# Performance work log

Hardware: AMD Instinct MI355X
Metric: run time of the kernel (lower is better)

The kernel has to match this reference:

```python
import jax, jax.numpy as jnp
import numpy as np

N_NODES = 100000
N_EDGES = 1_600_000
IN_CH = 128
HIDDEN = 128


def gcn_conv(x, src, dst, W, b):
    """PyG-style GCNConv: self-loops + symmetric deg^{-1/2} normalization."""
    n = x.shape[0]
    xw = x @ W  # [N, H]
    # degree on destination after adding self-loops (each node gets +1)
    deg = jax.ops.segment_sum(jnp.ones(src.shape[0], dtype=xw.dtype), dst,
                              num_segments=n) + 1.0
    dinv = jax.lax.rsqrt(deg)                      # deg^{-1/2}
    norm = dinv[src] * dinv[dst]                   # per-edge norm [E]
    agg = jax.ops.segment_sum(xw[src] * norm[:, None], dst, num_segments=n)
    # self-loop contribution: norm_ii = deg_i^{-1}
    return agg + xw * (1.0 / deg)[:, None] + b


def setup_inputs() -> dict:
    key = jax.random.key(0)
    ks = jax.random.split(key, 10)
    s = 0.05
    return {
        "node_features": jax.random.normal(ks[0], (N_NODES, IN_CH), dtype=jnp.float32),
        "edge_index": jax.random.randint(ks[1], (2, N_EDGES), 0, N_NODES, dtype=jnp.int32),
        "W1": jax.random.normal(ks[2], (IN_CH, HIDDEN), dtype=jnp.float32) * s,
        "b1": jnp.zeros((HIDDEN,), dtype=jnp.float32),
        "W2": jax.random.normal(ks[3], (HIDDEN, HIDDEN), dtype=jnp.float32) * s,
        "b2": jnp.zeros((HIDDEN,), dtype=jnp.float32),
        "fc1_w": jax.random.normal(ks[4], (2 * HIDDEN, HIDDEN), dtype=jnp.float32) * s,
        "fc1_b": jnp.zeros((HIDDEN,), dtype=jnp.float32),
        "fc2_w": jax.random.normal(ks[5], (HIDDEN, 1), dtype=jnp.float32) * s,
        "fc2_b": jnp.zeros((1,), dtype=jnp.float32),
    }


def reference(node_features, edge_index, W1, b1, W2, b2, fc1_w, fc1_b, fc2_w, fc2_b):
    src, dst = edge_index[0], edge_index[1]
    # two GCN layers (dropout is identity in eval mode)
    h = jax.nn.relu(gcn_conv(node_features, src, dst, W1, b1))
    h = jax.nn.relu(gcn_conv(h, src, dst, W2, b2))
    # edge feature head: gather endpoints, elementwise product/difference
    x = h[src]  # [E, H]
    y = h[dst]  # [E, H]
    edge_features = jnp.concatenate([x * y, x - y], axis=1)  # [E, 2H]
    z = jax.nn.relu(edge_features @ fc1_w + fc1_b)
    prob = jax.nn.sigmoid(z @ fc2_w + fc2_b)  # [E, 1]
    return prob
```

## Files before the change

### kernel.cpp

```cpp
#include <hip/hip_runtime.h>

#define THREADS 256

typedef __bf16    bf16x8 __attribute__((ext_vector_type(8)));
typedef __bf16    bf16x4 __attribute__((ext_vector_type(4)));
typedef _Float16  f16x8  __attribute__((ext_vector_type(8)));
typedef float     f32x4  __attribute__((ext_vector_type(4)));


__global__ __launch_bounds__(THREADS) void k_hist(const int* __restrict__ dst,
                                                  int* __restrict__ cnt, int E) {
    int e = blockIdx.x * THREADS + threadIdx.x;
    if (e < E) atomicAdd(&cnt[dst[e]], 1);
}

__global__ __launch_bounds__(THREADS) void k_dinv(const int* __restrict__ cnt,
                                                  float* __restrict__ dinv, int n) {
    int i = blockIdx.x * THREADS + threadIdx.x;
    if (i < n) dinv[i] = rsqrtf((float)cnt[i] + 1.0f);
}

__global__ __launch_bounds__(THREADS) void k_scan1(const int* __restrict__ cnt,
                                                   int* __restrict__ rowptr,
                                                   int* __restrict__ blockSums, int n) {
    __shared__ int part[THREADS];
    int tid = threadIdx.x;
    int base = blockIdx.x * 1024 + tid * 4;
    int v0 = (base + 0 < n) ? cnt[base + 0] : 0;
    int v1 = (base + 1 < n) ? cnt[base + 1] : 0;
    int v2 = (base + 2 < n) ? cnt[base + 2] : 0;
    int v3 = (base + 3 < n) ? cnt[base + 3] : 0;
    part[tid] = v0 + v1 + v2 + v3;
    __syncthreads();
    for (int off = 1; off < THREADS; off <<= 1) {
        int t = 0;
        if (tid >= off) t = part[tid - off];
        __syncthreads();
        if (tid >= off) part[tid] += t;
        __syncthreads();
    }
    int excl = (tid == 0) ? 0 : part[tid - 1];
    if (tid == THREADS - 1) blockSums[blockIdx.x] = part[THREADS - 1];
    int run = excl;
    if (base + 0 < n) rowptr[base + 0] = run; run += v0;
    if (base + 1 < n) rowptr[base + 1] = run; run += v1;
    if (base + 2 < n) rowptr[base + 2] = run; run += v2;
    if (base + 3 < n) rowptr[base + 3] = run;
}

__global__ __launch_bounds__(THREADS) void k_scan2(int* __restrict__ blockSums,
                                                   int* __restrict__ rowptr,
                                                   int nchunks, int n, int E) {
    __shared__ int part[THREADS];
    int tid = threadIdx.x;
    int v = (tid < nchunks) ? blockSums[tid] : 0;
    part[tid] = v;
    __syncthreads();
    for (int off = 1; off < THREADS; off <<= 1) {
        int t = 0;
        if (tid >= off) t = part[tid - off];
        __syncthreads();
        if (tid >= off) part[tid] += t;
        __syncthreads();
    }
    int excl = (tid == 0) ? 0 : part[tid - 1];
    if (tid < nchunks) blockSums[tid] = excl;
    if (tid == 0) rowptr[n] = E;
}

__global__ __launch_bounds__(THREADS) void k_scan3(int* __restrict__ rowptr,
                                                   const int* __restrict__ blockSums, int n) {
    int i = blockIdx.x * THREADS + threadIdx.x;
    if (i < n) rowptr[i] += blockSums[i >> 10];
}

__global__ __launch_bounds__(THREADS) void k_scatter(const int* __restrict__ src,
                                                     const int* __restrict__ dst,
                                                     const int* __restrict__ rowptr,
                                                     const float* __restrict__ dinv,
                                                     int* __restrict__ cursor,
                                                     int2* __restrict__ swPair,
                                                     int2* __restrict__ sdSorted,
                                                     int* __restrict__ edgePerm, int E) {
    int e = blockIdx.x * THREADS + threadIdx.x;
    if (e >= E) return;
    int d = dst[e];
    int s = src[e];
    int pos = rowptr[d] + atomicAdd(&cursor[d], 1);
    swPair[pos] = make_int2(s, __float_as_int(dinv[s]));
    sdSorted[pos] = make_int2(s, d);
    edgePerm[pos] = e;
}

__global__ __launch_bounds__(THREADS) void k_gemm128_f32(const float* __restrict__ A,
                                                         const float* __restrict__ B,
                                                         float* __restrict__ C,
                                                         __bf16* __restrict__ C16, int M) {
    __shared__ float4 As[64][8];
    __shared__ float4 Bs[32][32];

    int tid = threadIdx.x;
    int tx = tid & 31;
    int ty = tid >> 5;
    int row0 = blockIdx.x * 64;

    float4 acc[8];
#pragma unroll
    for (int i = 0; i < 8; i++) acc[i] = make_float4(0.f, 0.f, 0.f, 0.f);

    for (int k0 = 0; k0 < 128; k0 += 32) {
#pragma unroll
        for (int i = 0; i < 2; i++) {
            int idx = tid + i * 256;
            int r = idx >> 3, q = idx & 7;
            int row = row0 + r;
            float4 v = make_float4(0.f, 0.f, 0.f, 0.f);
            if (row < M) v = *(const float4*)(A + (size_t)row * 128 + k0 + q * 4);
            As[r][q] = v;
        }
#pragma unroll
        for (int i = 0; i < 4; i++) {
            int idx = tid + i * 256;
            int r = idx >> 5, c4 = idx & 31;
            Bs[r][c4] = *(const float4*)(B + (size_t)(k0 + r) * 128 + c4 * 4);
        }
        __syncthreads();

#pragma unroll
        for (int k4 = 0; k4 < 8; k4++) {
            float4 b0 = Bs[k4 * 4 + 0][tx];
            float4 b1 = Bs[k4 * 4 + 1][tx];
            float4 b2 = Bs[k4 * 4 + 2][tx];
            float4 b3 = Bs[k4 * 4 + 3][tx];
#pragma unroll
            for (int i = 0; i < 8; i++) {
                float4 a = As[ty * 8 + i][k4];
                acc[i].x = fmaf(a.x, b0.x, fmaf(a.y, b1.x, fmaf(a.z, b2.x, fmaf(a.w, b3.x, acc[i].x))));
                acc[i].y = fmaf(a.x, b0.y, fmaf(a.y, b1.y, fmaf(a.z, b2.y, fmaf(a.w, b3.y, acc[i].y))));
                acc[i].z = fmaf(a.x, b0.z, fmaf(a.y, b1.z, fmaf(a.z, b2.z, fmaf(a.w, b3.z, acc[i].z))));
                acc[i].w = fmaf(a.x, b0.w, fmaf(a.y, b1.w, fmaf(a.z, b2.w, fmaf(a.w, b3.w, acc[i].w))));
            }
        }
        __syncthreads();
    }

#pragma unroll
    for (int i = 0; i < 8; i++) {
        int row = row0 + ty * 8 + i;
        if (row < M) {
            *(float4*)(C + (size_t)row * 128 + tx * 4) = acc[i];
            bf16x4 c16;
            c16[0] = (__bf16)acc[i].x; c16[1] = (__bf16)acc[i].y;
            c16[2] = (__bf16)acc[i].z; c16[3] = (__bf16)acc[i].w;
            *(bf16x4*)(C16 + (size_t)row * 128 + tx * 4) = c16;
        }
    }
}

__global__ __launch_bounds__(THREADS) void k_gemm128_f16(const _Float16* __restrict__ A,
                                                         const float* __restrict__ B,
                                                         float* __restrict__ C,
                                                         __bf16* __restrict__ C16, int M) {
    __shared__ float4 As[64][8];
    __shared__ float4 Bs[32][32];

    int tid = threadIdx.x;
    int tx = tid & 31;
    int ty = tid >> 5;
    int row0 = blockIdx.x * 64;

    float4 acc[8];
#pragma unroll
    for (int i = 0; i < 8; i++) acc[i] = make_float4(0.f, 0.f, 0.f, 0.f);

    for (int k0 = 0; k0 < 128; k0 += 32) {
        {
            int r = tid >> 2, q = tid & 3;
            int row = row0 + r;
            f16x8 v;
            if (row < M) v = *(const f16x8*)(A + (size_t)row * 128 + k0 + q * 8);
            else { f16x8 z = {}; v = z; }
            float4 lo = make_float4((float)v[0], (float)v[1], (float)v[2], (float)v[3]);
            float4 hi = make_float4((float)v[4], (float)v[5], (float)v[6], (float)v[7]);
            As[r][q * 2] = lo;
            As[r][q * 2 + 1] = hi;
        }
#pragma unroll
        for (int i = 0; i < 4; i++) {
            int idx = tid + i * 256;
            int r = idx >> 5, c4 = idx & 31;
            Bs[r][c4] = *(const float4*)(B + (size_t)(k0 + r) * 128 + c4 * 4);
        }
        __syncthreads();

#pragma unroll
        for (int k4 = 0; k4 < 8; k4++) {
            float4 b0 = Bs[k4 * 4 + 0][tx];
            float4 b1 = Bs[k4 * 4 + 1][tx];
            float4 b2 = Bs[k4 * 4 + 2][tx];
            float4 b3 = Bs[k4 * 4 + 3][tx];
#pragma unroll
            for (int i = 0; i < 8; i++) {
                float4 a = As[ty * 8 + i][k4];
                acc[i].x = fmaf(a.x, b0.x, fmaf(a.y, b1.x, fmaf(a.z, b2.x, fmaf(a.w, b3.x, acc[i].x))));
                acc[i].y = fmaf(a.x, b0.y, fmaf(a.y, b1.y, fmaf(a.z, b2.y, fmaf(a.w, b3.y, acc[i].y))));
                acc[i].z = fmaf(a.x, b0.z, fmaf(a.y, b1.z, fmaf(a.z, b2.z, fmaf(a.w, b3.z, acc[i].z))));
                acc[i].w = fmaf(a.x, b0.w, fmaf(a.y, b1.w, fmaf(a.z, b2.w, fmaf(a.w, b3.w, acc[i].w))));
            }
        }
        __syncthreads();
    }

#pragma unroll
    for (int i = 0; i < 8; i++) {
        int row = row0 + ty * 8 + i;
        if (row < M) {
            *(float4*)(C + (size_t)row * 128 + tx * 4) = acc[i];
            bf16x4 c16;
            c16[0] = (__bf16)acc[i].x; c16[1] = (__bf16)acc[i].y;
            c16[2] = (__bf16)acc[i].z; c16[3] = (__bf16)acc[i].w;
            *(bf16x4*)(C16 + (size_t)row * 128 + tx * 4) = c16;
        }
    }
}

__global__ __launch_bounds__(THREADS) void k_gather_agg(const int* __restrict__ rowptr,
                                                        const int2* __restrict__ swPair,
                                                        const __bf16* __restrict__ xw16,
                                                        const float* __restrict__ xw,
                                                        const float* __restrict__ dinv,
                                                        const float* __restrict__ bias,
                                                        _Float16* __restrict__ h16, int n) {
    int node = blockIdx.x * 4 + (threadIdx.x >> 6);
    int lane = threadIdx.x & 63;
    int q = lane >> 4;
    int c = lane & 15;
    if (node >= n) return;
    int beg = rowptr[node], end = rowptr[node + 1];
    float di = dinv[node];

    float acc[8];
#pragma unroll
    for (int i = 0; i < 8; i++) acc[i] = 0.f;

    int j = beg;
    for (; j + 15 < end; j += 16) {
        int2 pw0 = swPair[j + q];
        int2 pw1 = swPair[j + 4 + q];
        int2 pw2 = swPair[j + 8 + q];
        int2 pw3 = swPair[j + 12 + q];
        bf16x8 v0 = *(const bf16x8*)(xw16 + (size_t)pw0.x * 128 + c * 8);
        bf16x8 v1 = *(const bf16x8*)(xw16 + (size_t)pw1.x * 128 + c * 8);
        bf16x8 v2 = *(const bf16x8*)(xw16 + (size_t)pw2.x * 128 + c * 8);
        bf16x8 v3 = *(const bf16x8*)(xw16 + (size_t)pw3.x * 128 + c * 8);
        float w0 = __int_as_float(pw0.y);
        float w1 = __int_as_float(pw1.y);
        float w2 = __int_as_float(pw2.y);
        float w3 = __int_as_float(pw3.y);
#pragma unroll
        for (int i = 0; i < 8; i++) {
            acc[i] = fmaf((float)v0[i], w0, acc[i]);
            acc[i] = fmaf((float)v1[i], w1, acc[i]);
            acc[i] = fmaf((float)v2[i], w2, acc[i]);
            acc[i] = fmaf((float)v3[i], w3, acc[i]);
        }
    }
    for (; j + 7 < end; j += 8) {
        int2 pw0 = swPair[j + q];
        int2 pw1 = swPair[j + 4 + q];
        bf16x8 v0 = *(const bf16x8*)(xw16 + (size_t)pw0.x * 128 + c * 8);
        bf16x8 v1 = *(const bf16x8*)(xw16 + (size_t)pw1.x * 128 + c * 8);
        float w0 = __int_as_float(pw0.y);
        float w1 = __int_as_float(pw1.y);
#pragma unroll
        for (int i = 0; i < 8; i++) {
            acc[i] = fmaf((float)v0[i], w0, acc[i]);
            acc[i] = fmaf((float)v1[i], w1, acc[i]);
        }
    }
    for (; j + 3 < end; j += 4) {
        int2 pw = swPair[j + q];
        bf16x8 v = *(const bf16x8*)(xw16 + (size_t)pw.x * 128 + c * 8);
        float w = __int_as_float(pw.y);
#pragma unroll
        for (int i = 0; i < 8; i++) acc[i] = fmaf((float)v[i], w, acc[i]);
    }
    int rem = end - j;
    if (q < rem) {
        int2 pw = swPair[j + q];
        bf16x8 v = *(const bf16x8*)(xw16 + (size_t)pw.x * 128 + c * 8);
        float w = __int_as_float(pw.y);
#pragma unroll
        for (int i = 0; i < 8; i++) acc[i] = fmaf((float)v[i], w, acc[i]);
    }

#pragma unroll
    for (int i = 0; i < 8; i++) {
        acc[i] += __shfl_xor(acc[i], 16);
        acc[i] += __shfl_xor(acc[i], 32);
    }

    if (q == 0) {
        float4 xv0 = *(const float4*)(xw + (size_t)node * 128 + c * 8);
        float4 xv1 = *(const float4*)(xw + (size_t)node * 128 + c * 8 + 4);
        float4 b0 = *(const float4*)(bias + c * 8);
        float4 b1 = *(const float4*)(bias + c * 8 + 4);
        float dd = di * di;
        float r[8];
        r[0] = fmaxf(fmaf(acc[0], di, fmaf(xv0.x, dd, b0.x)), 0.f);
        r[1] = fmaxf(fmaf(acc[1], di, fmaf(xv0.y, dd, b0.y)), 0.f);
        r[2] = fmaxf(fmaf(acc[2], di, fmaf(xv0.z, dd, b0.z)), 0.f);
        r[3] = fmaxf(fmaf(acc[3], di, fmaf(xv0.w, dd, b0.w)), 0.f);
        r[4] = fmaxf(fmaf(acc[4], di, fmaf(xv1.x, dd, b1.x)), 0.f);
        r[5] = fmaxf(fmaf(acc[5], di, fmaf(xv1.y, dd, b1.y)), 0.f);
        r[6] = fmaxf(fmaf(acc[6], di, fmaf(xv1.z, dd, b1.z)), 0.f);
        r[7] = fmaxf(fmaf(acc[7], di, fmaf(xv1.w, dd, b1.w)), 0.f);
        f16x8 r16;
#pragma unroll
        for (int i = 0; i < 8; i++) r16[i] = (_Float16)r[i];
        *(f16x8*)(h16 + (size_t)node * 128 + c * 8) = r16;
    }
}

__global__ __launch_bounds__(THREADS) void k_pack_b(const float* __restrict__ fc1w,
                                                    _Float16* __restrict__ bpack) {
    int t = blockIdx.x * THREADS + threadIdx.x;
    int lane = t & 63;
    int fi = t >> 6;
    int nt = fi & 7, ks = fi >> 3;
    int krow = ks * 32 + (lane >> 4) * 8;
    int col = nt * 16 + (lane & 15);
    f16x8 v;
#pragma unroll
    for (int i = 0; i < 8; i++) v[i] = (_Float16)fc1w[(size_t)(krow + i) * 128 + col];
    *(f16x8*)(bpack + (size_t)t * 8) = v;
}

__global__ __launch_bounds__(THREADS) void k_edge_head_mfma(const int2* __restrict__ sdSorted,
                                                            const int* __restrict__ edgePerm,
                                                            const _Float16* __restrict__ h16,
                                                            const _Float16* __restrict__ bpack,
                                                            const float* __restrict__ fc1b,
                                                            const float* __restrict__ fc2w,
                                                            const float* __restrict__ fc2b,
                                                            float* __restrict__ out, int E) {
    __shared__ _Float16 bsh[4096 * 8];

    int tid = threadIdx.x;
    {
        const int4* gsrc = (const int4*)bpack;
        int4* ldst = (int4*)bsh;
#pragma unroll
        for (int i = 0; i < 16; i++) ldst[tid + i * 256] = gsrc[tid + i * 256];
    }

    int w = tid >> 6;
    int lane = tid & 63;
    int m = lane & 15;
    int kg = lane >> 4;
    int n0 = lane & 15;
    int rowg = lane >> 4;
    int tile0 = blockIdx.x * 16 + w * 4;
    const f16x8* bfr = ((const f16x8*)bsh) + lane;
    float b2 = fc2b[0];

    float bb[8], ww[8];
#pragma unroll
    for (int nt = 0; nt < 8; nt++) {
        bb[nt] = fc1b[nt * 16 + n0];
        ww[nt] = fc2w[nt * 16 + n0];
    }

    auto LOAD = [&](int t, f16x8* xl, f16x8* yl) {
        int p = (tile0 + t) * 16 + m;
        int2 sd = (p < E) ? sdSorted[p] : make_int2(0, 0);
        const _Float16* px = h16 + (size_t)sd.x * 128 + kg * 8;
        const _Float16* py = h16 + (size_t)sd.y * 128 + kg * 8;
#pragma unroll
        for (int ks = 0; ks < 4; ks++) {
            xl[ks] = *(const f16x8*)(px + ks * 32);
            yl[ks] = *(const f16x8*)(py + ks * 32);
        }
    };

    auto COMPUTE = [&](int t, const f16x8* xl, const f16x8* yl) {
        f16x8 afrag[8];
#pragma unroll
        for (int ks = 0; ks < 4; ks++) {
            afrag[ks]     = xl[ks] * yl[ks];
            afrag[ks + 4] = xl[ks] - yl[ks];
        }
        f32x4 acc[8];
#pragma unroll
        for (int nt = 0; nt < 8; nt++) acc[nt] = (f32x4){bb[nt], bb[nt], bb[nt], bb[nt]};
#pragma unroll
        for (int ks = 0; ks < 8; ks++) {
#pragma unroll
            for (int nt = 0; nt < 8; nt++) {
                f16x8 b = bfr[(ks * 8 + nt) * 64];
                acc[nt] = __builtin_amdgcn_mfma_f32_16x16x32_f16(afrag[ks], b, acc[nt], 0, 0, 0);
            }
        }
        float partial[4] = {0.f, 0.f, 0.f, 0.f};
#pragma unroll
        for (int nt = 0; nt < 8; nt++) {
#pragma unroll
            for (int r = 0; r < 4; r++) {
                float z = fmaxf(acc[nt][r], 0.f);
                partial[r] = fmaf(z, ww[nt], partial[r]);
            }
        }
#pragma unroll
        for (int r = 0; r < 4; r++) {
            partial[r] += __shfl_xor(partial[r], 1);
            partial[r] += __shfl_xor(partial[r], 2);
            partial[r] += __shfl_xor(partial[r], 4);
            partial[r] += __shfl_xor(partial[r], 8);
        }
        if (n0 == 0) {
#pragma unroll
            for (int r = 0; r < 4; r++) {
                int qq = (tile0 + t) * 16 + rowg * 4 + r;
                if (qq < E) out[edgePerm[qq]] = 1.0f / (1.0f + expf(-(partial[r] + b2)));
            }
        }
    };

    f16x8 xa[4], ya[4], xb[4], yb[4];
    LOAD(0, xa, ya);
    __syncthreads();
    LOAD(1, xb, yb);
    COMPUTE(0, xa, ya);
    LOAD(2, xa, ya);
    COMPUTE(1, xb, yb);
    LOAD(3, xb, yb);
    COMPUTE(2, xa, ya);
    COMPUTE(3, xb, yb);
}

extern "C" void kernel_launch(void* const* d_in, const int* in_sizes, int n_in,
                              void* d_out, int out_size, void* d_ws, size_t ws_size,
                              hipStream_t stream) {
    const float* x    = (const float*)d_in[0];
    const int*   ei   = (const int*)d_in[1];
    const float* W1   = (const float*)d_in[2];
    const float* b1   = (const float*)d_in[3];
    const float* W2   = (const float*)d_in[4];
    const float* b2   = (const float*)d_in[5];
    const float* fc1w = (const float*)d_in[6];
    const float* fc1b = (const float*)d_in[7];
    const float* fc2w = (const float*)d_in[8];
    const float* fc2b = (const float*)d_in[9];

    int N = in_sizes[0] / 128;
    int E = in_sizes[1] / 2;
    const int* src = ei;
    const int* dst = ei + E;

    char* ws = (char*)d_ws;
    size_t off = 0;
    auto alloc = [&](size_t bytes) { char* p = ws + off; off += (bytes + 255) & ~(size_t)255; return p; };
    int*      cnt       = (int*)     alloc((size_t)N * 4);
    int*      rowptr    = (int*)     alloc(((size_t)N + 1) * 4);
    int*      cursor    = (int*)     alloc((size_t)N * 4);
    int*      blockSums = (int*)     alloc(256 * 4);
    int2*     swPair    = (int2*)    alloc((size_t)E * 8);
    int2*     sdSorted  = (int2*)    alloc((size_t)E * 8);
    int*      edgePerm  = (int*)     alloc((size_t)E * 4);
    float*    dinv      = (float*)   alloc((size_t)N * 4);
    _Float16* bpack     = (_Float16*)alloc((size_t)4096 * 8 * 2);
    float*    xw        = (float*)   alloc((size_t)N * 128 * 4);
    __bf16*   xw16      = (__bf16*)  alloc((size_t)N * 128 * 2);
    _Float16* h16       = (_Float16*)alloc((size_t)N * 128 * 2);

    int gN     = (N + THREADS - 1) / THREADS;
    int gE     = (E + THREADS - 1) / THREADS;
    int nchunk = (N + 1023) / 1024;
    int gGemm  = (N + 63) / 64;
    int gGath  = (N + 3) / 4;
    int gHead  = (E + 255) / 256;

    hipMemsetAsync(cnt, 0, (size_t)N * 4, stream);
    k_hist<<<gE, THREADS, 0, stream>>>(dst, cnt, E);
    k_dinv<<<gN, THREADS, 0, stream>>>(cnt, dinv, N);
    k_scan1<<<nchunk, THREADS, 0, stream>>>(cnt, rowptr, blockSums, N);
    k_scan2<<<1, THREADS, 0, stream>>>(blockSums, rowptr, nchunk, N, E);
    k_scan3<<<gN, THREADS, 0, stream>>>(rowptr, blockSums, N);
    hipMemsetAsync(cursor, 0, (size_t)N * 4, stream);
    k_scatter<<<gE, THREADS, 0, stream>>>(src, dst, rowptr, dinv, cursor,
                                          swPair, sdSorted, edgePerm, E);
    k_pack_b<<<16, THREADS, 0, stream>>>(fc1w, bpack);

    k_gemm128_f32<<<gGemm, THREADS, 0, stream>>>(x, W1, xw, xw16, N);
    k_gather_agg<<<gGath, THREADS, 0, stream>>>(rowptr, swPair, xw16, xw, dinv, b1, h16, N);

    k_gemm128_f16<<<gGemm, THREADS, 0, stream>>>(h16, W2, xw, xw16, N);
    k_gather_agg<<<gGath, THREADS, 0, stream>>>(rowptr, swPair, xw16, xw, dinv, b2, h16, N);

    k_edge_head_mfma<<<gHead, THREADS, 0, stream>>>(sdSorted, edgePerm,
                                                    h16, bpack, fc1b, fc2w, fc2b,
                                                    (float*)d_out, E);
}
```

Before: 560.8 us.

## Run node GEMMs on MFMA with prepacked fp16 weights and drop fp32 xw

Replaces the two FP32 SIMT 128x128 node GEMMs with MFMA 16x16x32 fp16 kernels that use weights prepacked into LDS by a new k_pack_w kernel. The fp32 xw output buffer is removed, so the gather-aggregate self-loop term now reads the bf16 copy. This cuts GEMM compute time and roughly 50MB of fp32 writes and reads per layer. In exchange, x and W are rounded to fp16 and the self-loop term uses bf16 precision. Output stores are scalar bf16 writes, which coalesce poorly.

Result: faster. 494.7 us (-11.8%).

```diff
diff --git a/kernel.cpp b/kernel.cpp
--- a/kernel.cpp
+++ b/kernel.cpp
@@ -3,7 +3,6 @@
 #define THREADS 256
 
 typedef __bf16    bf16x8 __attribute__((ext_vector_type(8)));
-typedef __bf16    bf16x4 __attribute__((ext_vector_type(4)));
 typedef _Float16  f16x8  __attribute__((ext_vector_type(8)));
 typedef float     f32x4  __attribute__((ext_vector_type(4)));
 
@@ -92,134 +91,132 @@
     edgePerm[pos] = e;
 }
 
-__global__ __launch_bounds__(THREADS) void k_gemm128_f32(const float* __restrict__ A,
-                                                         const float* __restrict__ B,
-                                                         float* __restrict__ C,
-                                                         __bf16* __restrict__ C16, int M) {
-    __shared__ float4 As[64][8];
-    __shared__ float4 Bs[32][32];
-
+__global__ __launch_bounds__(THREADS) void k_pack_w(const float* __restrict__ W1,
+                                                    const float* __restrict__ W2,
+                                                    _Float16* __restrict__ wp1,
+                                                    _Float16* __restrict__ wp2) {
+    int t = blockIdx.x * THREADS + threadIdx.x;
+    const float* W = (t < 2048) ? W1 : W2;
+    _Float16* wp = (t < 2048) ? wp1 : wp2;
+    int tt = t & 2047;
+    int lane = tt & 63;
+    int fi = tt >> 6;
+    int nt = fi & 7, ks = fi >> 3;
+    int krow = ks * 32 + (lane >> 4) * 8;
+    int col = nt * 16 + (lane & 15);
+    f16x8 v;
+#pragma unroll
+    for (int i = 0; i < 8; i++) v[i] = (_Float16)W[(size_t)(krow + i) * 128 + col];
+    *(f16x8*)(wp + (size_t)tt * 8) = v;
+}
+
+__global__ __launch_bounds__(THREADS) void k_gemm_mfma_f32(const float* __restrict__ A,
+                                                           const _Float16* __restrict__ wpack,
+                                                           __bf16* __restrict__ C16, int M) {
+    __shared__ _Float16 wsh[2048 * 8];
     int tid = threadIdx.x;
-    int tx = tid & 31;
-    int ty = tid >> 5;
-    int row0 = blockIdx.x * 64;
-
-    float4 acc[8];
-#pragma unroll
-    for (int i = 0; i < 8; i++) acc[i] = make_float4(0.f, 0.f, 0.f, 0.f);
-
-    for (int k0 = 0; k0 < 128; k0 += 32) {
-#pragma unroll
-        for (int i = 0; i < 2; i++) {
-            int idx = tid + i * 256;
-            int r = idx >> 3, q = idx & 7;
-            int row = row0 + r;
-            float4 v = make_float4(0.f, 0.f, 0.f, 0.f);
-            if (row < M) v = *(const float4*)(A + (size_t)row * 128 + k0 + q * 4);
-            As[r][q] = v;
-        }
-#pragma unroll
-        for (int i = 0; i < 4; i++) {
-            int idx = tid + i * 256;
-            int r = idx >> 5, c4 = idx & 31;
-            Bs[r][c4] = *(const float4*)(B + (size_t)(k0 + r) * 128 + c4 * 4);
-        }
-        __syncthreads();
-
-#pragma unroll
-        for (int k4 = 0; k4 < 8; k4++) {
-            float4 b0 = Bs[k4 * 4 + 0][tx];
-            float4 b1 = Bs[k4 * 4 + 1][tx];
-            float4 b2 = Bs[k4 * 4 + 2][tx];
-            float4 b3 = Bs[k4 * 4 + 3][tx];
-#pragma unroll
-            for (int i = 0; i < 8; i++) {
-                float4 a = As[ty * 8 + i][k4];
-                acc[i].x = fmaf(a.x, b0.x, fmaf(a.y, b1.x, fmaf(a.z, b2.x, fmaf(a.w, b3.x, acc[i].x))));
-                acc[i].y = fmaf(a.x, b0.y, fmaf(a.y, b1.y, fmaf(a.z, b2.y, fmaf(a.w, b3.y, acc[i].y))));
-                acc[i].z = fmaf(a.x, b0.z, fmaf(a.y, b1.z, fmaf(a.z, b2.z, fmaf(a.w, b3.z, acc[i].z))));
-                acc[i].w = fmaf(a.x, b0.w, fmaf(a.y, b1.w, fmaf(a.z, b2.w, fmaf(a.w, b3.w, acc[i].w))));
-            }
-        }
-        __syncthreads();
-    }
-
-#pragma unroll
-    for (int i = 0; i < 8; i++) {
-        int row = row0 + ty * 8 + i;
+    {
+        const int4* g = (const int4*)wpack;
+        int4* l = (int4*)wsh;
+#pragma unroll
+        for (int i = 0; i < 8; i++) l[tid + i * 256] = g[tid + i * 256];
+    }
+    int w = tid >> 6, lane = tid & 63;
+    int m = lane & 15, kg = lane >> 4;
+    int n0 = lane & 15, rowg = lane >> 4;
+    int tile0 = blockIdx.x * 16 + w * 4;
+    __syncthreads();
+    const f16x8* wfr = ((const f16x8*)wsh) + lane;
+
+    for (int t = 0; t < 4; t++) {
+        int row = (tile0 + t) * 16 + m;
+        f16x8 a[4];
         if (row < M) {
-            *(float4*)(C + (size_t)row * 128 + tx * 4) = acc[i];
-            bf16x4 c16;
-            c16[0] = (__bf16)acc[i].x; c16[1] = (__bf16)acc[i].y;
-            c16[2] = (__bf16)acc[i].z; c16[3] = (__bf16)acc[i].w;
-            *(bf16x4*)(C16 + (size_t)row * 128 + tx * 4) = c16;
-        }
-    }
-}
-
-__global__ __launch_bounds__(THREADS) void k_gemm128_f16(const _Float16* __restrict__ A,
-                                                         const float* __restrict__ B,
-                                                         float* __restrict__ C,
-                                                         __bf16* __restrict__ C16, int M) {
-    __shared__ float4 As[64][8];
-    __shared__ float4 Bs[32][32];
-
+            const float* pa = A + (size_t)row * 128 + kg * 8;
+#pragma unroll
+            for (int ks = 0; ks < 4; ks++) {
+                float4 lo = *(const float4*)(pa + ks * 32);
+                float4 hi = *(const float4*)(pa + ks * 32 + 4);
+                f16x8 v;
+                v[0] = (_Float16)lo.x; v[1] = (_Float16)lo.y;
+                v[2] = (_Float16)lo.z; v[3] = (_Float16)lo.w;
+                v[4] = (_Float16)hi.x; v[5] = (_Float16)hi.y;
+                v[6] = (_Float16)hi.z; v[7] = (_Float16)hi.w;
+                a[ks] = v;
+            }
+        } else {
+#pragma unroll
+            for (int ks = 0; ks < 4; ks++) { f16x8 z = {}; a[ks] = z; }
+        }
+        f32x4 acc[8];
+#pragma unroll
+        for (int i = 0; i < 8; i++) acc[i] = (f32x4){0.f, 0.f, 0.f, 0.f};
+#pragma unroll
+        for (int ks = 0; ks < 4; ks++) {
+#pragma unroll
+            for (int nt = 0; nt < 8; nt++) {
+                f16x8 b = wfr[(ks * 8 + nt) * 64];
+                acc[nt] = __builtin_amdgcn_mfma_f32_16x16x32_f16(a[ks], b, acc[nt], 0, 0, 0);
+            }
+        }
+#pragma unroll
+        for (int nt = 0; nt < 8; nt++) {
+#pragma unroll
+            for (int r = 0; r < 4; r++) {
+                int ro = (tile0 + t) * 16 + rowg * 4 + r;
+                if (ro < M) C16[(size_t)ro * 128 + nt * 16 + n0] = (__bf16)acc[nt][r];
+            }
+        }
+    }
+}
+
+__global__ __launch_bounds__(THREADS) void k_gemm_mfma_f16(const _Float16* __restrict__ A,
+                                                           const _Float16* __restrict__ wpack,
+                                                           __bf16* __restrict__ C16, int M) {
+    __shared__ _Float16 wsh[2048 * 8];
     int tid = threadIdx.x;
-    int tx = tid & 31;
-    int ty = tid >> 5;
-    int row0 = blockIdx.x * 64;
-
-    float4 acc[8];
-#pragma unroll
-    for (int i = 0; i < 8; i++) acc[i] = make_float4(0.f, 0.f, 0.f, 0.f);
-
-    for (int k0 = 0; k0 < 128; k0 += 32) {
-        {
-            int r = tid >> 2, q = tid & 3;
-            int row = row0 + r;
-            f16x8 v;
-            if (row < M) v = *(const f16x8*)(A + (size_t)row * 128 + k0 + q * 8);
-            else { f16x8 z = {}; v = z; }
-            float4 lo = make_float4((float)v[0], (float)v[1], (float)v[2], (float)v[3]);
-            float4 hi = make_float4((float)v[4], (float)v[5], (float)v[6], (float)v[7]);
-            As[r][q * 2] = lo;
-            As[r][q * 2 + 1] = hi;
-        }
-#pragma unroll
-        for (int i = 0; i < 4; i++) {
-            int idx = tid + i * 256;
-            int r = idx >> 5, c4 = idx & 31;
-            Bs[r][c4] = *(const float4*)(B + (size_t)(k0 + r) * 128 + c4 * 4);
-        }
-        __syncthreads();
-
-#pragma unroll
-        for (int k4 = 0; k4 < 8; k4++) {
-            float4 b0 = Bs[k4 * 4 + 0][tx];
-            float4 b1 = Bs[k4 * 4 + 1][tx];
-            float4 b2 = Bs[k4 * 4 + 2][tx];
-            float4 b3 = Bs[k4 * 4 + 3][tx];
-#pragma unroll
-            for (int i = 0; i < 8; i++) {
-                float4 a = As[ty * 8 + i][k4];
-                acc[i].x = fmaf(a.x, b0.x, fmaf(a.y, b1.x, fmaf(a.z, b2.x, fmaf(a.w, b3.x, acc[i].x))));
-                acc[i].y = fmaf(a.x, b0.y, fmaf(a.y, b1.y, fmaf(a.z, b2.y, fmaf(a.w, b3.y, acc[i].y))));
-                acc[i].z = fmaf(a.x, b0.z, fmaf(a.y, b1.z, fmaf(a.z, b2.z, fmaf(a.w, b3.z, acc[i].z))));
-                acc[i].w = fmaf(a.x, b0.w, fmaf(a.y, b1.w, fmaf(a.z, b2.w, fmaf(a.w, b3.w, acc[i].w))));
-            }
-        }
-        __syncthreads();
-    }
-
-#pragma unroll
-    for (int i = 0; i < 8; i++) {
-        int row = row0 + ty * 8 + i;
+    {
+        const int4* g = (const int4*)wpack;
+        int4* l = (int4*)wsh;
+#pragma unroll
+        for (int i = 0; i < 8; i++) l[tid + i * 256] = g[tid + i * 256];
+    }
+    int w = tid >> 6, lane = tid & 63;
+    int m = lane & 15, kg = lane >> 4;
+    int n0 = lane & 15, rowg = lane >> 4;
+    int tile0 = blockIdx.x * 16 + w * 4;
+    __syncthreads();
+    const f16x8* wfr = ((const f16x8*)wsh) + lane;
+
+    for (int t = 0; t < 4; t++) {
+        int row = (tile0 + t) * 16 + m;
+        f16x8 a[4];
         if (row < M) {
-            *(float4*)(C + (size_t)row * 128 + tx * 4) = acc[i];
-            bf16x4 c16;
-            c16[0] = (__bf16)acc[i].x; c16[1] = (__bf16)acc[i].y;
-            c16[2] = (__bf16)acc[i].z; c16[3] = (__bf16)acc[i].w;
-            *(bf16x4*)(C16 + (size_t)row * 128 + tx * 4) = c16;
+            const _Float16* pa = A + (size_t)row * 128 + kg * 8;
+#pragma unroll
+            for (int ks = 0; ks < 4; ks++) a[ks] = *(const f16x8*)(pa + ks * 32);
+        } else {
+#pragma unroll
+            for (int ks = 0; ks < 4; ks++) { f16x8 z = {}; a[ks] = z; }
+        }
+        f32x4 acc[8];
+#pragma unroll
+        for (int i = 0; i < 8; i++) acc[i] = (f32x4){0.f, 0.f, 0.f, 0.f};
+#pragma unroll
+        for (int ks = 0; ks < 4; ks++) {
+#pragma unroll
+            for (int nt = 0; nt < 8; nt++) {
+                f16x8 b = wfr[(ks * 8 + nt) * 64];
+                acc[nt] = __builtin_amdgcn_mfma_f32_16x16x32_f16(a[ks], b, acc[nt], 0, 0, 0);
+            }
+        }
+#pragma unroll
+        for (int nt = 0; nt < 8; nt++) {
+#pragma unroll
+            for (int r = 0; r < 4; r++) {
+                int ro = (tile0 + t) * 16 + rowg * 4 + r;
+                if (ro < M) C16[(size_t)ro * 128 + nt * 16 + n0] = (__bf16)acc[nt][r];
+            }
         }
     }
 }
@@ -227,7 +224,6 @@
 __global__ __launch_bounds__(THREADS) void k_gather_agg(const int* __restrict__ rowptr,
                                                         const int2* __restrict__ swPair,
                                                         const __bf16* __restrict__ xw16,
-                                                        const float* __restrict__ xw,
                                                         const float* __restrict__ dinv,
                                                         const float* __restrict__ bias,
                                                         _Float16* __restrict__ h16, int n) {
@@ -301,23 +297,17 @@
     }
 
     if (q == 0) {
-        float4 xv0 = *(const float4*)(xw + (size_t)node * 128 + c * 8);
-        float4 xv1 = *(const float4*)(xw + (size_t)node * 128 + c * 8 + 4);
+        bf16x8 sv = *(const bf16x8*)(xw16 + (size_t)node * 128 + c * 8);
         float4 b0 = *(const float4*)(bias + c * 8);
         float4 b1 = *(const float4*)(bias + c * 8 + 4);
+        float bb[8] = {b0.x, b0.y, b0.z, b0.w, b1.x, b1.y, b1.z, b1.w};
         float dd = di * di;
-        float r[8];
-        r[0] = fmaxf(fmaf(acc[0], di, fmaf(xv0.x, dd, b0.x)), 0.f);
-        r[1] = fmaxf(fmaf(acc[1], di, fmaf(xv0.y, dd, b0.y)), 0.f);
-        r[2] = fmaxf(fmaf(acc[2], di, fmaf(xv0.z, dd, b0.z)), 0.f);
-        r[3] = fmaxf(fmaf(acc[3], di, fmaf(xv0.w, dd, b0.w)), 0.f);
-        r[4] = fmaxf(fmaf(acc[4], di, fmaf(xv1.x, dd, b1.x)), 0.f);
-        r[5] = fmaxf(fmaf(acc[5], di, fmaf(xv1.y, dd, b1.y)), 0.f);
-        r[6] = fmaxf(fmaf(acc[6], di, fmaf(xv1.z, dd, b1.z)), 0.f);
-        r[7] = fmaxf(fmaf(acc[7], di, fmaf(xv1.w, dd, b1.w)), 0.f);
         f16x8 r16;
 #pragma unroll
-        for (int i = 0; i < 8; i++) r16[i] = (_Float16)r[i];
+        for (int i = 0; i < 8; i++) {
+            float r = fmaf(acc[i], di, fmaf((float)sv[i], dd, bb[i]));
+            r16[i] = (_Float16)fmaxf(r, 0.f);
+        }
         *(f16x8*)(h16 + (size_t)node * 128 + c * 8) = r16;
     }
 }
@@ -469,14 +459,16 @@
     int*      edgePerm  = (int*)     alloc((size_t)E * 4);
     float*    dinv      = (float*)   alloc((size_t)N * 4);
     _Float16* bpack     = (_Float16*)alloc((size_t)4096 * 8 * 2);
-    float*    xw        = (float*)   alloc((size_t)N * 128 * 4);
+    _Float16* wp1       = (_Float16*)alloc((size_t)2048 * 8 * 2);
+    _Float16* wp2       = (_Float16*)alloc((size_t)2048 * 8 * 2);
     __bf16*   xw16      = (__bf16*)  alloc((size_t)N * 128 * 2);
     _Float16* h16       = (_Float16*)alloc((size_t)N * 128 * 2);
 
     int gN     = (N + THREADS - 1) / THREADS;
     int gE     = (E + THREADS - 1) / THREADS;
     int nchunk = (N + 1023) / 1024;
-    int gGemm  = (N + 63) / 64;
+    int nTileG = (N + 15) / 16;
+    int gGemm  = (nTileG + 15) / 16;
     int gGath  = (N + 3) / 4;
     int gHead  = (E + 255) / 256;
 
@@ -490,12 +482,13 @@
     k_scatter<<<gE, THREADS, 0, stream>>>(src, dst, rowptr, dinv, cursor,
                                           swPair, sdSorted, edgePerm, E);
     k_pack_b<<<16, THREADS, 0, stream>>>(fc1w, bpack);
-
-    k_gemm128_f32<<<gGemm, THREADS, 0, stream>>>(x, W1, xw, xw16, N);
-    k_gather_agg<<<gGath, THREADS, 0, stream>>>(rowptr, swPair, xw16, xw, dinv, b1, h16, N);
-
-    k_gemm128_f16<<<gGemm, THREADS, 0, stream>>>(h16, W2, xw, xw16, N);
-    k_gather_agg<<<gGath, THREADS, 0, stream>>>(rowptr, swPair, xw16, xw, dinv, b2, h16, N);
+    k_pack_w<<<16, THREADS, 0, stream>>>(W1, W2, wp1, wp2);
+
+    k_gemm_mfma_f32<<<gGemm, THREADS, 0, stream>>>(x, wp1, xw16, N);
+    k_gather_agg<<<gGath, THREADS, 0, stream>>>(rowptr, swPair, xw16, dinv, b1, h16, N);
+
+    k_gemm_mfma_f16<<<gGemm, THREADS, 0, stream>>>(h16, wp2, xw16, N);
+    k_gather_agg<<<gGath, THREADS, 0, stream>>>(rowptr, swPair, xw16, dinv, b2, h16, N);
 
     k_edge_head_mfma<<<gHead, THREADS, 0, stream>>>(sdSorted, edgePerm,
                                                     h16, bpack, fc1b, fc2w, fc2b,
```
